# Performance work log

Hardware: AMD Instinct MI355X
Metric: run time of the kernel (lower is better)

## Reference

```python
import jax, jax.numpy as jnp
import numpy as np
from jax.scipy.special import logsumexp

PAD = 0  # NlpContext().padding_idx


def setup_inputs() -> dict:
    key = jax.random.key(0)
    k1, k2, k3 = jax.random.split(key, 3)
    B, S, L = 4, 1024, 128
    pred = jax.random.normal(k1, (B, S, L), dtype=jnp.float32)
    # labels in [1, L): no token equals PAD -> mask is all-zero, non_pad_length == S
    gt = jax.random.randint(k2, (B, S), 1, L)
    transition = jax.random.normal(k3, (L, L), dtype=jnp.float32)
    return {"pred": pred, "gt": gt, "transition": transition}


def _crf_loss(pred, gt, transition):
    # Faithful translation of LinearCRFLoss.forward (including the alpha
    # broadcasting behaviour of the original torch loop).
    mask = (gt == PAD).astype(pred.dtype)                 # (B,S), all-zero here
    logp = jax.nn.log_softmax(pred, -1) * (1.0 - mask)[:, :, None]  # (B,S,L)
    trans = jax.nn.log_softmax(transition, -1)            # (L,L)

    # posterior_t[b,i,j] = log_softmax_j( logp[b,t,i] + trans[i,j]*(1-mask[b,t]) )
    post = jax.nn.log_softmax(
        logp[:, :, :, None] + trans[None, None] * (1.0 - mask)[:, :, None, None],
        axis=-1,
    )  # (B,S,L,L)

    # t = 1: alpha has shape (B,L,1) in the original -> broadcasts over 'to'
    # axis j; reduce (logsumexp) over the 'from' axis i.
    alpha = logsumexp(post[:, 1] + logp[:, 0, :, None], axis=1)  # (B,L)
    # t >= 2: alpha has shape (B,1,L) in the original -> broadcasts over the
    # 'from' axis i, so it factors out of the logsumexp:
    #   alpha_t[j] = alpha_{t-1}[j] + lse_i post_t[i,j]
    # which telescopes into a single sum over t (identical math, vectorized).
    alpha = alpha + logsumexp(post[:, 2:], axis=2).sum(axis=1)   # (B,L)
    forward_score = logsumexp(alpha, axis=-1)                    # (B,)

    # gold path score (non_pad_length == S since there is no padding)
    emit = jnp.take_along_axis(logp, gt[:, :, None], axis=2)[..., 0].sum(-1)  # (B,)
    tr = trans[gt[:, :-1], gt[:, 1:]].sum(-1)                                  # (B,)
    gold = emit + tr
    return -(gold - forward_score).mean()


def reference(pred, gt, transition):
    return _crf_loss(pred, gt, transition)
```

## Files before the change

kernel.cpp:

```cpp
#include <hip/hip_runtime.h>
#include <hip/hip_bf16.h>
#include <math.h>

#define BB 4
#define SS 1024
#define LL 128


__global__ __launch_bounds__(256) void crf_rows_kernel(
    const float* __restrict__ pred,
    const int* __restrict__ gt,
    const float* __restrict__ transition,
    float* __restrict__ ws_part,
    float* __restrict__ ws_elp,
    float* __restrict__ ws_trans)
{
    const int wave = threadIdx.x >> 6;
    const int lane = threadIdx.x & 63;
    const int row0 = blockIdx.x * 16;

    float2 v[4];
    #pragma unroll
    for (int it = 0; it < 4; ++it) {
        const int r = row0 + it * 4 + wave;
        v[it] = ((const float2*)(pred + (size_t)r * LL))[lane];
    }
    float gval[4] = {0.f, 0.f, 0.f, 0.f};
    if (lane == 0) {
        int gi[4];
        #pragma unroll
        for (int it = 0; it < 4; ++it) gi[it] = gt[row0 + it * 4 + wave];
        #pragma unroll
        for (int it = 0; it < 4; ++it)
            gval[it] = pred[(size_t)(row0 + it * 4 + wave) * LL + gi[it]];
    }

    float local = 0.f;
    #pragma unroll
    for (int it = 0; it < 4; ++it) {
        float m = fmaxf(v[it].x, v[it].y);
        #pragma unroll
        for (int off = 32; off > 0; off >>= 1) m = fmaxf(m, __shfl_xor(m, off));
        float s = __expf(v[it].x - m) + __expf(v[it].y - m);
        #pragma unroll
        for (int off = 32; off > 0; off >>= 1) s += __shfl_xor(s, off);
        const float lse = m + __logf(s);

        if (lane == 0) local += gval[it] - lse;

        if (it == 0 && wave == 0 && (blockIdx.x & 63) == 0) {
            const int b = blockIdx.x >> 6;
            ws_elp[b * LL + 2 * lane]     = __expf(v[0].x - lse);
            ws_elp[b * LL + 2 * lane + 1] = __expf(v[0].y - lse);
        }
    }

    if (blockIdx.x < LL && wave == 0) {
        const float2 tv = ((const float2*)(transition + blockIdx.x * LL))[lane];
        float m = fmaxf(tv.x, tv.y);
        #pragma unroll
        for (int off = 32; off > 0; off >>= 1) m = fmaxf(m, __shfl_xor(m, off));
        float s = __expf(tv.x - m) + __expf(tv.y - m);
        #pragma unroll
        for (int off = 32; off > 0; off >>= 1) s += __shfl_xor(s, off);
        const float lse = m + __logf(s);
        float2 o; o.x = tv.x - lse; o.y = tv.y - lse;
        ((float2*)(ws_trans + blockIdx.x * LL))[lane] = o;
    }

    __shared__ float red[4];
    if (lane == 0) red[wave] = local;
    __syncthreads();
    if (threadIdx.x == 0)
        ws_part[blockIdx.x] = red[0] + red[1] + red[2] + red[3];
}

#define PADL (LL + 4)
__global__ __launch_bounds__(512) void crf_finish_kernel(
    const int* __restrict__ gt,
    const float* __restrict__ ws_part,
    const float* __restrict__ ws_elp,
    const float* __restrict__ ws_trans,
    float* __restrict__ out)
{
    __shared__ float tr_s[LL][PADL];
    __shared__ float elp_s[BB][LL];
    __shared__ float pc[4][LL];
    __shared__ float pa[4][BB][LL];
    __shared__ float emit_s[BB];
    __shared__ float wred[8];
    __shared__ float fm[8], fs[8];

    const int tid  = threadIdx.x;
    const int lane = tid & 63;
    const int wave = tid >> 6;

    #pragma unroll
    for (int k = 0; k < 8; ++k) {
        const int e = (tid + k * 512) * 4;
        const int i = e >> 7, j = e & (LL - 1);
        *(float4*)&tr_s[i][j] = ((const float4*)ws_trans)[e >> 2];
    }
    elp_s[tid >> 7][tid & (LL - 1)] = ws_elp[tid];
    if (wave < BB) {
        float p = ws_part[wave * 64 + lane];
        #pragma unroll
        for (int off = 32; off > 0; off >>= 1) p += __shfl_xor(p, off);
        if (lane == 0) emit_s[wave] = p;
    }
    __syncthreads();

    {
        const int sub = tid >> 7;
        const int j   = tid & (LL - 1);
        float sc = 0.f, s0 = 0.f, s1 = 0.f, s2 = 0.f, s3 = 0.f;
        #pragma unroll
        for (int k = 0; k < 32; ++k) {
            const int i = sub * 32 + k;
            const float e = __expf(tr_s[i][j]);
            sc += e;
            s0 += e * elp_s[0][i];
            s1 += e * elp_s[1][i];
            s2 += e * elp_s[2][i];
            s3 += e * elp_s[3][i];
        }
        pc[sub][j] = sc;
        pa[sub][0][j] = s0; pa[sub][1][j] = s1;
        pa[sub][2][j] = s2; pa[sub][3][j] = s3;
    }
    {
        const int b  = tid >> 7;
        const int t0 = tid & (LL - 1);
        const int* gtb = gt + b * SS;
        float g = 0.f;
        for (int t = t0; t < SS - 1; t += LL)
            g += tr_s[gtb[t]][gtb[t + 1]];
        #pragma unroll
        for (int off = 32; off > 0; off >>= 1) g += __shfl_xor(g, off);
        if (lane == 0) wred[wave] = g;
    }
    __syncthreads();

    {
        const int b = tid >> 7;
        const int j = tid & (LL - 1);
        const float csum = pc[0][j] + pc[1][j] + pc[2][j] + pc[3][j];
        const float asum = pa[0][b][j] + pa[1][b][j] + pa[2][b][j] + pa[3][b][j];
        const float alpha = __logf(asum) + (float)(SS - 2) * __logf(csum);

        float wm = alpha;
        #pragma unroll
        for (int off = 32; off > 0; off >>= 1) wm = fmaxf(wm, __shfl_xor(wm, off));
        float wsum = __expf(alpha - wm);
        #pragma unroll
        for (int off = 32; off > 0; off >>= 1) wsum += __shfl_xor(wsum, off);
        if (lane == 0) { fm[wave] = wm; fs[wave] = wsum; }
    }
    __syncthreads();

    if (tid < BB) {
        const float m0 = fm[2 * tid], m1 = fm[2 * tid + 1];
        const float mm = fmaxf(m0, m1);
        const float fwd = mm + __logf(fs[2 * tid] * __expf(m0 - mm)
                                    + fs[2 * tid + 1] * __expf(m1 - mm));
        const float gold = wred[2 * tid] + wred[2 * tid + 1];
        fm[tid] = emit_s[tid] + gold - fwd;
    }
    __syncthreads();
    if (tid == 0)
        out[0] = -(fm[0] + fm[1] + fm[2] + fm[3]) * (1.0f / BB);
}

extern "C" void kernel_launch(void* const* d_in, const int* in_sizes, int n_in,
                              void* d_out, int out_size, void* d_ws, size_t ws_size,
                              hipStream_t stream) {
    const float* pred       = (const float*)d_in[0];
    const int*   gt         = (const int*)d_in[1];
    const float* transition = (const float*)d_in[2];
    float* out = (float*)d_out;

    float* ws_part  = (float*)d_ws;
    float* ws_elp   = ws_part + 256;
    float* ws_trans = ws_part + 768;

    crf_rows_kernel<<<(BB * SS) / 16, 256, 0, stream>>>(
        pred, gt, transition, ws_part, ws_elp, ws_trans);
    crf_finish_kernel<<<1, 512, 0, stream>>>(gt, ws_part, ws_elp, ws_trans, out);
}
```

Measured before the change: 64.49 us.

## Fuse row and finish kernels using per-block flags and a spinning final block

Merges the two launches into one kernel. Every block publishes its partial sums and then sets a release flag. Block 0 spin-waits on all 256 flags and then runs the transition/forward/gold reduction itself, which removes the second launch and its gap. It also gets the gold emission with a wave shuffle instead of a scattered load and stages gt in shared memory. The flags are never reset, so on repeated calls block 0 may read the previous call's workspace before this call's writes land. It also relies on all blocks being co-resident, and it gives every block a large LDS allocation.

```diff
diff --git a/kernel.cpp b/kernel.cpp
--- a/kernel.cpp
+++ b/kernel.cpp
@@ -5,35 +5,45 @@
 #define BB 4
 #define SS 1024
 #define LL 128
-
-
-__global__ __launch_bounds__(256) void crf_rows_kernel(
+#define PADL (LL + 4)
+#define MAGIC 0x5CA1AB1Eu
+
+
+__global__ __launch_bounds__(256) void crf_fused_kernel(
     const float* __restrict__ pred,
     const int* __restrict__ gt,
     const float* __restrict__ transition,
+    unsigned int* __restrict__ ws_flags,
     float* __restrict__ ws_part,
     float* __restrict__ ws_elp,
-    float* __restrict__ ws_trans)
+    float* __restrict__ ws_trans,
+    float* __restrict__ out)
 {
-    const int wave = threadIdx.x >> 6;
-    const int lane = threadIdx.x & 63;
-    const int row0 = blockIdx.x * 16;
-
+    __shared__ float tr_s[LL][PADL];
+    __shared__ int   gt_s[BB * SS];
+    __shared__ float elp_s[BB][LL];
+    __shared__ float pc[2][LL];
+    __shared__ float pa[2][BB][LL];
+    __shared__ float alpha_s[BB][LL];
+    __shared__ float redA[4];
+    __shared__ float emit_s[BB], gold_s[BB], fwd_s[BB];
+
+    const int tid  = threadIdx.x;
+    const int wave = tid >> 6;
+    const int lane = tid & 63;
+    const int blk  = blockIdx.x;
+    const int row0 = blk * 16;
+
+    int gi[4];
+    #pragma unroll
+    for (int it = 0; it < 4; ++it) gi[it] = gt[row0 + it * 4 + wave];
     float2 v[4];
     #pragma unroll
-    for (int it = 0; it < 4; ++it) {
-        const int r = row0 + it * 4 + wave;
-        v[it] = ((const float2*)(pred + (size_t)r * LL))[lane];
-    }
-    float gval[4] = {0.f, 0.f, 0.f, 0.f};
-    if (lane == 0) {
-        int gi[4];
-        #pragma unroll
-        for (int it = 0; it < 4; ++it) gi[it] = gt[row0 + it * 4 + wave];
-        #pragma unroll
-        for (int it = 0; it < 4; ++it)
-            gval[it] = pred[(size_t)(row0 + it * 4 + wave) * LL + gi[it]];
-    }
+    for (int it = 0; it < 4; ++it)
+        v[it] = ((const float2*)(pred + (size_t)(row0 + it * 4 + wave) * LL))[lane];
+    const bool do_trans = (blk < LL) && (wave == 0);
+    float2 tv;
+    if (do_trans) tv = ((const float2*)(transition + blk * LL))[lane];
 
     float local = 0.f;
     #pragma unroll
@@ -46,17 +56,18 @@
         for (int off = 32; off > 0; off >>= 1) s += __shfl_xor(s, off);
         const float lse = m + __logf(s);
 
-        if (lane == 0) local += gval[it] - lse;
-
-        if (it == 0 && wave == 0 && (blockIdx.x & 63) == 0) {
-            const int b = blockIdx.x >> 6;
+        const int g = gi[it];
+        const float hold = (g & 1) ? v[it].y : v[it].x;
+        local += __shfl(hold, g >> 1) - lse;
+
+        if (it == 0 && wave == 0 && (blk & 63) == 0) {
+            const int b = blk >> 6;
             ws_elp[b * LL + 2 * lane]     = __expf(v[0].x - lse);
             ws_elp[b * LL + 2 * lane + 1] = __expf(v[0].y - lse);
         }
     }
 
-    if (blockIdx.x < LL && wave == 0) {
-        const float2 tv = ((const float2*)(transition + blockIdx.x * LL))[lane];
+    if (do_trans) {
         float m = fmaxf(tv.x, tv.y);
         #pragma unroll
         for (int off = 32; off > 0; off >>= 1) m = fmaxf(m, __shfl_xor(m, off));
@@ -65,44 +76,42 @@
         for (int off = 32; off > 0; off >>= 1) s += __shfl_xor(s, off);
         const float lse = m + __logf(s);
         float2 o; o.x = tv.x - lse; o.y = tv.y - lse;
-        ((float2*)(ws_trans + blockIdx.x * LL))[lane] = o;
-    }
-
-    __shared__ float red[4];
-    if (lane == 0) red[wave] = local;
-    __syncthreads();
-    if (threadIdx.x == 0)
-        ws_part[blockIdx.x] = red[0] + red[1] + red[2] + red[3];
-}
-
-#define PADL (LL + 4)
-__global__ __launch_bounds__(512) void crf_finish_kernel(
-    const int* __restrict__ gt,
-    const float* __restrict__ ws_part,
-    const float* __restrict__ ws_elp,
-    const float* __restrict__ ws_trans,
-    float* __restrict__ out)
-{
-    __shared__ float tr_s[LL][PADL];
-    __shared__ float elp_s[BB][LL];
-    __shared__ float pc[4][LL];
-    __shared__ float pa[4][BB][LL];
-    __shared__ float emit_s[BB];
-    __shared__ float wred[8];
-    __shared__ float fm[8], fs[8];
-
-    const int tid  = threadIdx.x;
-    const int lane = tid & 63;
-    const int wave = tid >> 6;
-
-    #pragma unroll
-    for (int k = 0; k < 8; ++k) {
-        const int e = (tid + k * 512) * 4;
-        const int i = e >> 7, j = e & (LL - 1);
-        *(float4*)&tr_s[i][j] = ((const float4*)ws_trans)[e >> 2];
-    }
-    elp_s[tid >> 7][tid & (LL - 1)] = ws_elp[tid];
-    if (wave < BB) {
+        ((float2*)(ws_trans + blk * LL))[lane] = o;
+    }
+
+    if (lane == 0) redA[wave] = local;
+    __syncthreads();
+    if (tid == 0) {
+        ws_part[blk] = redA[0] + redA[1] + redA[2] + redA[3];
+        __threadfence();
+        __hip_atomic_store(&ws_flags[blk], MAGIC, __ATOMIC_RELEASE,
+                           __HIP_MEMORY_SCOPE_AGENT);
+    }
+    if (blk != 0) return;
+
+    #pragma unroll
+    for (int k = 0; k < 4; ++k) {
+        const int q = tid + k * 256;
+        ((int4*)gt_s)[q] = ((const int4*)gt)[q];
+    }
+    while (__hip_atomic_load(&ws_flags[tid], __ATOMIC_ACQUIRE,
+                             __HIP_MEMORY_SCOPE_AGENT) != MAGIC)
+        __builtin_amdgcn_s_sleep(1);
+    __syncthreads();
+    __threadfence();
+
+    #pragma unroll
+    for (int k = 0; k < 16; ++k) {
+        const int q = tid + k * 256;
+        const int e = q * 4;
+        *(float4*)&tr_s[e >> 7][e & (LL - 1)] = ((const float4*)ws_trans)[q];
+    }
+    #pragma unroll
+    for (int k = 0; k < 2; ++k) {
+        const int e = tid + k * 256;
+        elp_s[e >> 7][e & (LL - 1)] = ws_elp[e];
+    }
+    {
         float p = ws_part[wave * 64 + lane];
         #pragma unroll
         for (int off = 32; off > 0; off >>= 1) p += __shfl_xor(p, off);
@@ -114,9 +123,9 @@
         const int sub = tid >> 7;
         const int j   = tid & (LL - 1);
         float sc = 0.f, s0 = 0.f, s1 = 0.f, s2 = 0.f, s3 = 0.f;
-        #pragma unroll
-        for (int k = 0; k < 32; ++k) {
-            const int i = sub * 32 + k;
+        #pragma unroll 8
+        for (int k = 0; k < 64; ++k) {
+            const int i = sub * 64 + k;
             const float e = __expf(tr_s[i][j]);
             sc += e;
             s0 += e * elp_s[0][i];
@@ -129,46 +138,50 @@
         pa[sub][2][j] = s2; pa[sub][3][j] = s3;
     }
     {
-        const int b  = tid >> 7;
-        const int t0 = tid & (LL - 1);
-        const int* gtb = gt + b * SS;
+        const int* gtb = gt_s + wave * SS;
         float g = 0.f;
-        for (int t = t0; t < SS - 1; t += LL)
+        for (int t = lane; t < SS - 1; t += 64)
             g += tr_s[gtb[t]][gtb[t + 1]];
         #pragma unroll
         for (int off = 32; off > 0; off >>= 1) g += __shfl_xor(g, off);
-        if (lane == 0) wred[wave] = g;
-    }
-    __syncthreads();
-
-    {
-        const int b = tid >> 7;
+        if (lane == 0) gold_s[wave] = g;
+    }
+    __syncthreads();
+
+    {
+        const int s = tid >> 7;
         const int j = tid & (LL - 1);
-        const float csum = pc[0][j] + pc[1][j] + pc[2][j] + pc[3][j];
-        const float asum = pa[0][b][j] + pa[1][b][j] + pa[2][b][j] + pa[3][b][j];
-        const float alpha = __logf(asum) + (float)(SS - 2) * __logf(csum);
-
-        float wm = alpha;
-        #pragma unroll
-        for (int off = 32; off > 0; off >>= 1) wm = fmaxf(wm, __shfl_xor(wm, off));
-        float wsum = __expf(alpha - wm);
-        #pragma unroll
-        for (int off = 32; off > 0; off >>= 1) wsum += __shfl_xor(wsum, off);
-        if (lane == 0) { fm[wave] = wm; fs[wave] = wsum; }
-    }
-    __syncthreads();
-
-    if (tid < BB) {
-        const float m0 = fm[2 * tid], m1 = fm[2 * tid + 1];
-        const float mm = fmaxf(m0, m1);
-        const float fwd = mm + __logf(fs[2 * tid] * __expf(m0 - mm)
-                                    + fs[2 * tid + 1] * __expf(m1 - mm));
-        const float gold = wred[2 * tid] + wred[2 * tid + 1];
-        fm[tid] = emit_s[tid] + gold - fwd;
-    }
-    __syncthreads();
-    if (tid == 0)
-        out[0] = -(fm[0] + fm[1] + fm[2] + fm[3]) * (1.0f / BB);
+        const float csum = pc[0][j] + pc[1][j];
+        const float lc   = (float)(SS - 2) * __logf(csum);
+        #pragma unroll
+        for (int b = 0; b < 2; ++b) {
+            const int bb = s + 2 * b;
+            const float asum = pa[0][bb][j] + pa[1][bb][j];
+            alpha_s[bb][j] = __logf(asum) + lc;
+        }
+    }
+    __syncthreads();
+
+    {
+        const float a0 = alpha_s[wave][lane];
+        const float a1 = alpha_s[wave][lane + 64];
+        float m = fmaxf(a0, a1);
+        #pragma unroll
+        for (int off = 32; off > 0; off >>= 1) m = fmaxf(m, __shfl_xor(m, off));
+        float s = __expf(a0 - m) + __expf(a1 - m);
+        #pragma unroll
+        for (int off = 32; off > 0; off >>= 1) s += __shfl_xor(s, off);
+        if (lane == 0) fwd_s[wave] = m + __logf(s);
+    }
+    __syncthreads();
+
+    if (tid == 0) {
+        float tot = 0.f;
+        #pragma unroll
+        for (int b = 0; b < BB; ++b)
+            tot += emit_s[b] + gold_s[b] - fwd_s[b];
+        out[0] = -tot * (1.0f / BB);
+    }
 }
 
 extern "C" void kernel_launch(void* const* d_in, const int* in_sizes, int n_in,
@@ -179,11 +192,11 @@
     const float* transition = (const float*)d_in[2];
     float* out = (float*)d_out;
 
-    float* ws_part  = (float*)d_ws;
-    float* ws_elp   = ws_part + 256;
-    float* ws_trans = ws_part + 768;
-
-    crf_rows_kernel<<<(BB * SS) / 16, 256, 0, stream>>>(
-        pred, gt, transition, ws_part, ws_elp, ws_trans);
-    crf_finish_kernel<<<1, 512, 0, stream>>>(gt, ws_part, ws_elp, ws_trans, out);
+    unsigned int* ws_flags = (unsigned int*)d_ws;
+    float* ws_part  = (float*)d_ws + 256;
+    float* ws_elp   = (float*)d_ws + 512;
+    float* ws_trans = (float*)d_ws + 1024;
+
+    crf_fused_kernel<<<256, 256, 0, stream>>>(
+        pred, gt, transition, ws_flags, ws_part, ws_elp, ws_trans, out);
 }
```

After: 70.88 us. 9.9% more time.
